# Kernel tuning notes

Measured on AMD Instinct MI355X. Metric: run time of the kernel, lower is better.

Reference implementation:

```python
import jax, jax.numpy as jnp
import numpy as np

NUM_FREQ = 32
MAX_POS = 10000.0
COORD_DIM = 3
EMB_DIM = COORD_DIM * NUM_FREQ * 2  # 192
KIN = 2 * EMB_DIM                   # 384
C = 32
T = 4
N_Y = 50000
N_X = 32768
K = 8
E = N_X * K
MLP_DIMS = [KIN, 128, 256, 128, C]


def sinusoidal_embed(p):
    # transformer-style sinusoidal embedding: [n, d] -> [n, d*NUM_FREQ*2]
    freqs = (1.0 / MAX_POS) ** (jnp.arange(NUM_FREQ, dtype=p.dtype) / NUM_FREQ)
    ang = p[..., None] * freqs                       # [n, d, nf]
    emb = jnp.stack([jnp.sin(ang), jnp.cos(ang)], axis=-1)  # [n, d, nf, 2]
    return emb.reshape(p.shape[0], -1)


def setup_inputs() -> dict:
    key = jax.random.key(0)
    ks = jax.random.split(key, 16)
    inp = {
        "y": jax.random.uniform(ks[0], (N_Y, COORD_DIM), dtype=jnp.float32),
        "x": jax.random.uniform(ks[1], (N_X, COORD_DIM), dtype=jnp.float32),
        "f_y": jax.random.normal(ks[2], (T, N_Y, C), dtype=jnp.float32),
        "neighbors_index": jax.random.randint(ks[3], (E,), 0, N_Y, dtype=jnp.int64),
    }
    # channel MLP params: 384 -> 128 -> 256 -> 128 -> 32, gelu between layers
    for i in range(4):
        fan_in, fan_out = MLP_DIMS[i], MLP_DIMS[i + 1]
        s = 1.0 / np.sqrt(fan_in)
        inp[f"W{i}"] = jax.random.uniform(ks[4 + 2 * i], (fan_in, fan_out), jnp.float32, -s, s)
        inp[f"b{i}"] = jax.random.uniform(ks[5 + 2 * i], (fan_out,), jnp.float32, -s, s)
    return inp


def reference(y, x, f_y, neighbors_index, W0, b0, W1, b1, W2, b2, W3, b3):
    n_x = x.shape[0]
    k = neighbors_index.shape[0] // n_x
    y_emb = sinusoidal_embed(y)            # [n_y, 192]
    x_emb = sinusoidal_embed(x)            # [n_x, 192]
    rep = y_emb[neighbors_index]           # [E, 192] gather per edge
    slf = jnp.repeat(x_emb, k, axis=0)     # [E, 192] query embedding per edge
    h = jnp.concatenate([rep, slf], axis=-1)  # [E, 384]
    h = jax.nn.gelu(h @ W0 + b0)
    h = jax.nn.gelu(h @ W1 + b1)
    h = jax.nn.gelu(h @ W2 + b2)
    kern = h @ W3 + b3                     # [E, C] kernel values
    in_feat = f_y[:, neighbors_index, :]   # [T, E, C] gathered source features
    prod = kern[None, :, :] * in_feat      # linear transform: k(x,y) * f(y)
    # reduction='sum' over each query's neighborhood (uniform K segments)
    out = prod.reshape(f_y.shape[0], n_x, k, -1).sum(axis=2)  # [T, n_x, C]
    return out
```

## Files before the change

kernel.cpp:

```cpp
#include <hip/hip_runtime.h>
#include <stdint.h>

#define EMB_DIM 192
#define CDIM 32
#define TDIM 4
#define N_Y 50000
#define N_X 32768
#define KNBR 8
#define ECNT (N_X*KNBR)

#define H1S 134
#define H2S 262
#define KS  33
#define ES  200

#define PREP_TW 272
#define PREP_Y0 PREP_TW
#define PREP_X0 (PREP_TW + 782)
#define PREP_NB (PREP_TW + 782 + 512)

typedef __attribute__((ext_vector_type(8))) short bf16x8;
typedef __attribute__((ext_vector_type(4))) float f32x4;

static __device__ __forceinline__ short f2bf(float f){
  unsigned u = __float_as_uint(f);
  return (short)((u + 0x7FFFu) >> 16);
}
static __device__ __forceinline__ unsigned pk_bf16(float lo, float hi){
  return ((__float_as_uint(lo) + 0x7FFFu) >> 16) |
         ((((__float_as_uint(hi) + 0x7FFFu) >> 16)) << 16);
}
static __device__ __forceinline__ float geluf(float x){
  float x2 = x * x;
  float u  = __builtin_fmaf(0.044715f, x2, 1.0f);
  float p  = x * -1.5957691216057308f;
  float e  = __expf(p * u);
  return x * __builtin_amdgcn_rcpf(1.0f + e);
}

__global__ __launch_bounds__(256, 2) void prep_all(
    const float* __restrict__ ypts, const float* __restrict__ xpts,
    const float* __restrict__ W0, const float* __restrict__ b0,
    const float* __restrict__ W1, const float* __restrict__ W2,
    const float* __restrict__ W3,
    short* __restrict__ w1t, short* __restrict__ w2t, short* __restrict__ w3t,
    short* __restrict__ c_y, float* __restrict__ c_x)
{
  const int tid = threadIdx.x;
  if (blockIdx.x < PREP_TW) {
    int id = blockIdx.x * 256 + tid;
    if (id < 32768) {
      int n = id >> 7, k = id & 127;
      w1t[id] = f2bf(W1[k * 256 + n]);
    } else if (id < 65536) {
      int loc = id - 32768; int n = loc >> 8, k = loc & 255;
      w2t[loc] = f2bf(W2[k * 128 + n]);
    } else if (id < 69632) {
      int loc = id - 65536; int n = loc >> 7, k = loc & 127;
      w3t[loc] = f2bf(W3[k * 32 + n]);
    }
    return;
  }

  __shared__ __attribute__((aligned(16))) short s_e[64 * ES];
  const bool isY = blockIdx.x < PREP_X0;
  const int row0 = isY ? (blockIdx.x - PREP_Y0) * 64 : (blockIdx.x - PREP_X0) * 64;
  const int wave = tid >> 6, lane = tid & 63;
  const int quad = lane >> 4, l15 = lane & 15;
  const float* W0h = W0 + (isY ? 0 : 192 * 128);

  short bv[2][48];
  #pragma unroll
  for (int nt = 0; nt < 2; ++nt) {
    int n = wave * 32 + nt * 16 + l15;
    #pragma unroll
    for (int ch = 0; ch < 6; ++ch)
      #pragma unroll
      for (int j = 0; j < 8; ++j)
        bv[nt][ch * 8 + j] = f2bf(W0h[(size_t)(ch * 32 + quad * 8 + j) * 128 + n]);
  }

  {
    const int r = tid >> 2, q = tid & 3;
    const int grow = row0 + r;
    const bool valid = isY ? (grow < N_Y) : true;
    const float* src = isY ? (ypts + (size_t)grow * 3) : (xpts + (size_t)grow * 3);
    float c[3] = {0.f, 0.f, 0.f};
    if (valid) { c[0] = src[0]; c[1] = src[1]; c[2] = src[2]; }
    #pragma unroll
    for (int j = 0; j < 24; ++j) {
      int p = q * 24 + j;
      int d = p >> 5, i = p & 31;
      float f = __expf(-0.28782313662425575f * (float)i);
      float rev = c[d] * f * 0.15915494309189535f;
      float s  = __builtin_amdgcn_sinf(rev);
      float co = __builtin_amdgcn_cosf(rev);
      *(unsigned*)&s_e[r * ES + d * 64 + 2 * i] = pk_bf16(s, co);
    }
  }
  __syncthreads();

  f32x4 acc[4][2];
  #pragma unroll
  for (int mt = 0; mt < 4; ++mt)
    #pragma unroll
    for (int nt = 0; nt < 2; ++nt) acc[mt][nt] = (f32x4){0.f, 0.f, 0.f, 0.f};
  #pragma unroll
  for (int ch = 0; ch < 6; ++ch) {
    bf16x8 a[4];
    #pragma unroll
    for (int mt = 0; mt < 4; ++mt)
      a[mt] = *(const bf16x8*)&s_e[(mt * 16 + l15) * ES + ch * 32 + quad * 8];
    #pragma unroll
    for (int mt = 0; mt < 4; ++mt)
      #pragma unroll
      for (int nt = 0; nt < 2; ++nt)
        acc[mt][nt] = __builtin_amdgcn_mfma_f32_16x16x32_bf16(
            a[mt], *(const bf16x8*)&bv[nt][ch * 8], acc[mt][nt], 0, 0, 0);
  }
  #pragma unroll
  for (int nt = 0; nt < 2; ++nt) {
    int col = wave * 32 + nt * 16 + l15;
    float bias = isY ? 0.f : b0[col];
    #pragma unroll
    for (int mt = 0; mt < 4; ++mt)
      #pragma unroll
      for (int rg = 0; rg < 4; ++rg) {
        int grow = row0 + mt * 16 + quad * 4 + rg;
        if (isY) { if (grow < N_Y) c_y[(size_t)grow * 128 + col] = f2bf(acc[mt][nt][rg]); }
        else     { c_x[(size_t)grow * 128 + col] = acc[mt][nt][rg] + bias; }
      }
  }
}

__global__ __launch_bounds__(256, 3) void fused_edge(
    const short* __restrict__ c_y, const float* __restrict__ c_x,
    const int* __restrict__ nidx, const float* __restrict__ f_y,
    const short* __restrict__ w1t, const float* __restrict__ b1,
    const short* __restrict__ w2t, const float* __restrict__ b2,
    const short* __restrict__ w3t, const float* __restrict__ b3,
    float* __restrict__ out)
{
  __shared__ __attribute__((aligned(16))) char smem[50688];
  short* s_h2   = (short*)smem;
  float* s_kern = (float*)smem;
  short* s_h1   = (short*)(smem + 33536);

  const int tid  = threadIdx.x;
  const int e0   = blockIdx.x * 64;
  const int wave = tid >> 6, lane = tid & 63;
  const int quad = lane >> 4, l15 = lane & 15;

  {
    const int r = tid >> 2, q = tid & 3;
    const int idx = nidx[e0 + r];
    const uint4*  cyp = (const uint4*)(c_y + (size_t)idx * 128 + q * 32);
    const float4* cxp = (const float4*)(c_x + (size_t)((e0 + r) >> 3) * 128 + q * 32);
    uint4  cyv[4];
    float4 cxv[8];
    #pragma unroll
    for (int i = 0; i < 4; ++i) cyv[i] = cyp[i];
    #pragma unroll
    for (int i = 0; i < 8; ++i) cxv[i] = cxp[i];
    const float* cxa = (const float*)cxv;
    const unsigned* cya = (const unsigned*)cyv;
    unsigned pk[16];
    #pragma unroll
    for (int jj = 0; jj < 16; ++jj) {
      unsigned u = cya[jj];
      float lo = __uint_as_float(u << 16)         + cxa[2 * jj];
      float hi = __uint_as_float(u & 0xffff0000u) + cxa[2 * jj + 1];
      pk[jj] = pk_bf16(geluf(lo), geluf(hi));
    }
    uint4* dst = (uint4*)&s_h1[r * H1S + q * 32];
    #pragma unroll
    for (int jj = 0; jj < 4; ++jj)
      dst[jj] = *(uint4*)&pk[jj * 4];
  }
  __syncthreads();

  {
    f32x4 acc1[4][4];
    #pragma unroll
    for (int mt = 0; mt < 4; ++mt)
      #pragma unroll
      for (int nt = 0; nt < 4; ++nt) acc1[mt][nt] = (f32x4){0.f, 0.f, 0.f, 0.f};
    #pragma unroll
    for (int ch = 0; ch < 4; ++ch) {
      bf16x8 a[4], b[4];
      #pragma unroll
      for (int mt = 0; mt < 4; ++mt)
        a[mt] = *(const bf16x8*)&s_h1[(mt * 16 + l15) * H1S + ch * 32 + quad * 8];
      #pragma unroll
      for (int nt = 0; nt < 4; ++nt)
        b[nt] = *(const bf16x8*)&w1t[(size_t)(wave * 64 + nt * 16 + l15) * 128 + ch * 32 + quad * 8];
      #pragma unroll
      for (int mt = 0; mt < 4; ++mt)
        #pragma unroll
        for (int nt = 0; nt < 4; ++nt)
          acc1[mt][nt] = __builtin_amdgcn_mfma_f32_16x16x32_bf16(a[mt], b[nt], acc1[mt][nt], 0, 0, 0);
    }
    #pragma unroll
    for (int nt = 0; nt < 4; ++nt) {
      int col = wave * 64 + nt * 16 + l15;
      float bias = b1[col];
      #pragma unroll
      for (int mt = 0; mt < 4; ++mt)
        #pragma unroll
        for (int rg = 0; rg < 4; ++rg) {
          int row = mt * 16 + quad * 4 + rg;
          s_h2[row * H2S + col] = f2bf(geluf(acc1[mt][nt][rg] + bias));
        }
    }
  }
  __syncthreads();

  {
    f32x4 acc2[4][2];
    #pragma unroll
    for (int mt = 0; mt < 4; ++mt)
      #pragma unroll
      for (int nt = 0; nt < 2; ++nt) acc2[mt][nt] = (f32x4){0.f, 0.f, 0.f, 0.f};
    #pragma unroll
    for (int ch = 0; ch < 8; ++ch) {
      bf16x8 a[4], b[2];
      #pragma unroll
      for (int mt = 0; mt < 4; ++mt)
        a[mt] = *(const bf16x8*)&s_h2[(mt * 16 + l15) * H2S + ch * 32 + quad * 8];
      #pragma unroll
      for (int nt = 0; nt < 2; ++nt)
        b[nt] = *(const bf16x8*)&w2t[(size_t)(wave * 32 + nt * 16 + l15) * 256 + ch * 32 + quad * 8];
      #pragma unroll
      for (int mt = 0; mt < 4; ++mt)
        #pragma unroll
        for (int nt = 0; nt < 2; ++nt)
          acc2[mt][nt] = __builtin_amdgcn_mfma_f32_16x16x32_bf16(a[mt], b[nt], acc2[mt][nt], 0, 0, 0);
    }
    #pragma unroll
    for (int nt = 0; nt < 2; ++nt) {
      int col = wave * 32 + nt * 16 + l15;
      float bias = b2[col];
      #pragma unroll
      for (int mt = 0; mt < 4; ++mt)
        #pragma unroll
        for (int rg = 0; rg < 4; ++rg) {
          int row = mt * 16 + quad * 4 + rg;
          s_h1[row * H1S + col] = f2bf(geluf(acc2[mt][nt][rg] + bias));
        }
    }
  }
  __syncthreads();

  {
    f32x4 acc3[2];
    acc3[0] = (f32x4){0.f, 0.f, 0.f, 0.f};
    acc3[1] = (f32x4){0.f, 0.f, 0.f, 0.f};
    #pragma unroll
    for (int ch = 0; ch < 4; ++ch) {
      bf16x8 a3 = *(const bf16x8*)&s_h1[(wave * 16 + l15) * H1S + ch * 32 + quad * 8];
      #pragma unroll
      for (int nt = 0; nt < 2; ++nt) {
        bf16x8 b3f = *(const bf16x8*)&w3t[(size_t)(nt * 16 + l15) * 128 + ch * 32 + quad * 8];
        acc3[nt] = __builtin_amdgcn_mfma_f32_16x16x32_bf16(a3, b3f, acc3[nt], 0, 0, 0);
      }
    }
    #pragma unroll
    for (int nt = 0; nt < 2; ++nt) {
      int col = nt * 16 + l15;
      float bias = b3[col];
      #pragma unroll
      for (int rg = 0; rg < 4; ++rg) {
        int row = wave * 16 + quad * 4 + rg;
        s_kern[row * KS + col] = acc3[nt][rg] + bias;
      }
    }
  }
  __syncthreads();

  {
    const int xloc = tid >> 5;
    const int c    = tid & 31;
    float acc[TDIM] = {0.f, 0.f, 0.f, 0.f};
    const int ebase = xloc * 8;
    #pragma unroll
    for (int j = 0; j < KNBR; ++j) {
      float kv = s_kern[(ebase + j) * KS + c];
      int idx = nidx[e0 + ebase + j];
      const float* fp = f_y + (size_t)idx * CDIM + c;
      #pragma unroll
      for (int t = 0; t < TDIM; ++t)
        acc[t] += kv * fp[(size_t)t * N_Y * CDIM];
    }
    const int xg = blockIdx.x * 8 + xloc;
    #pragma unroll
    for (int t = 0; t < TDIM; ++t)
      out[((size_t)t * N_X + xg) * CDIM + c] = acc[t];
  }
}

extern "C" void kernel_launch(void* const* d_in, const int* in_sizes, int n_in,
                              void* d_out, int out_size, void* d_ws, size_t ws_size,
                              hipStream_t stream)
{
  const float* y   = (const float*)d_in[0];
  const float* x   = (const float*)d_in[1];
  const float* f_y = (const float*)d_in[2];
  const int*  nidx = (const int*)d_in[3];
  const float* W0 = (const float*)d_in[4];  const float* b0 = (const float*)d_in[5];
  const float* W1 = (const float*)d_in[6];  const float* b1 = (const float*)d_in[7];
  const float* W2 = (const float*)d_in[8];  const float* b2 = (const float*)d_in[9];
  const float* W3 = (const float*)d_in[10]; const float* b3 = (const float*)d_in[11];

  char* ws = (char*)d_ws;
  short* c_y  = (short*)(ws + 0);
  float* c_x  = (float*)(ws + 12800000);
  short* w1t  = (short*)(ws + 29577216);
  short* w2t  = (short*)(ws + 29642752);
  short* w3t  = (short*)(ws + 29708288);

  hipLaunchKernelGGL(prep_all, dim3(PREP_NB), dim3(256), 0, stream,
                     y, x, W0, b0, W1, W2, W3, w1t, w2t, w3t, c_y, c_x);
  hipLaunchKernelGGL(fused_edge, dim3(ECNT / 64), dim3(256), 0, stream,
                     c_y, c_x, nidx, f_y, w1t, b1, w2t, b2, w3t, b3, (float*)d_out);
}
```

Measured before the change: 239.4 us.

## Prefetch f_y gathers and MLP weight fragments early to overlap latency

The random f_y gathers for the final reduction are now issued at kernel start and held in registers (32 floats per thread) across the whole MLP. The per-layer weight fragments are loaded into registers ahead of each MFMA loop, and the next layer's weights are issued before the current layer's GELU epilogue. The aim is to hide global-memory latency behind MFMA compute. The cost is much higher register pressure under launch_bounds(256,3), which may cause spills or lower occupancy.

```diff
diff --git a/kernel.cpp b/kernel.cpp
--- a/kernel.cpp
+++ b/kernel.cpp
@@ -151,17 +151,40 @@
   const int wave = tid >> 6, lane = tid & 63;
   const int quad = lane >> 4, l15 = lane & 15;
 
+  const int xloc = tid >> 5;
+  const int cc   = tid & 31;
+  int fidx[KNBR];
+  #pragma unroll
+  for (int j = 0; j < KNBR; ++j) fidx[j] = nidx[e0 + xloc * 8 + j];
+
+  const int r = tid >> 2, q = tid & 3;
+  const int idx = nidx[e0 + r];
+  const uint4*  cyp = (const uint4*)(c_y + (size_t)idx * 128 + q * 32);
+  const float4* cxp = (const float4*)(c_x + (size_t)((e0 + r) >> 3) * 128 + q * 32);
+  uint4  cyv[4];
+  float4 cxv[8];
+  #pragma unroll
+  for (int i = 0; i < 4; ++i) cyv[i] = cyp[i];
+  #pragma unroll
+  for (int i = 0; i < 8; ++i) cxv[i] = cxp[i];
+
+  bf16x8 b1f[4][4];
+  #pragma unroll
+  for (int ch = 0; ch < 4; ++ch)
+    #pragma unroll
+    for (int nt = 0; nt < 4; ++nt)
+      b1f[ch][nt] = *(const bf16x8*)&w1t[(size_t)(wave * 64 + nt * 16 + l15) * 128 + ch * 32 + quad * 8];
+
+  float fv[KNBR][TDIM];
+  #pragma unroll
+  for (int j = 0; j < KNBR; ++j) {
+    const float* fp = f_y + (size_t)fidx[j] * CDIM + cc;
+    #pragma unroll
+    for (int t = 0; t < TDIM; ++t)
+      fv[j][t] = fp[(size_t)t * (N_Y * CDIM)];
+  }
+
   {
-    const int r = tid >> 2, q = tid & 3;
-    const int idx = nidx[e0 + r];
-    const uint4*  cyp = (const uint4*)(c_y + (size_t)idx * 128 + q * 32);
-    const float4* cxp = (const float4*)(c_x + (size_t)((e0 + r) >> 3) * 128 + q * 32);
-    uint4  cyv[4];
-    float4 cxv[8];
-    #pragma unroll
-    for (int i = 0; i < 4; ++i) cyv[i] = cyp[i];
-    #pragma unroll
-    for (int i = 0; i < 8; ++i) cxv[i] = cxp[i];
     const float* cxa = (const float*)cxv;
     const unsigned* cya = (const unsigned*)cyv;
     unsigned pk[16];
@@ -179,75 +202,81 @@
   }
   __syncthreads();
 
-  {
-    f32x4 acc1[4][4];
-    #pragma unroll
-    for (int mt = 0; mt < 4; ++mt)
-      #pragma unroll
-      for (int nt = 0; nt < 4; ++nt) acc1[mt][nt] = (f32x4){0.f, 0.f, 0.f, 0.f};
-    #pragma unroll
-    for (int ch = 0; ch < 4; ++ch) {
-      bf16x8 a[4], b[4];
-      #pragma unroll
-      for (int mt = 0; mt < 4; ++mt)
-        a[mt] = *(const bf16x8*)&s_h1[(mt * 16 + l15) * H1S + ch * 32 + quad * 8];
+  f32x4 acc1[4][4];
+  #pragma unroll
+  for (int mt = 0; mt < 4; ++mt)
+    #pragma unroll
+    for (int nt = 0; nt < 4; ++nt) acc1[mt][nt] = (f32x4){0.f, 0.f, 0.f, 0.f};
+  #pragma unroll
+  for (int ch = 0; ch < 4; ++ch) {
+    bf16x8 a[4];
+    #pragma unroll
+    for (int mt = 0; mt < 4; ++mt)
+      a[mt] = *(const bf16x8*)&s_h1[(mt * 16 + l15) * H1S + ch * 32 + quad * 8];
+    #pragma unroll
+    for (int mt = 0; mt < 4; ++mt)
       #pragma unroll
       for (int nt = 0; nt < 4; ++nt)
-        b[nt] = *(const bf16x8*)&w1t[(size_t)(wave * 64 + nt * 16 + l15) * 128 + ch * 32 + quad * 8];
-      #pragma unroll
-      for (int mt = 0; mt < 4; ++mt)
-        #pragma unroll
-        for (int nt = 0; nt < 4; ++nt)
-          acc1[mt][nt] = __builtin_amdgcn_mfma_f32_16x16x32_bf16(a[mt], b[nt], acc1[mt][nt], 0, 0, 0);
-    }
-    #pragma unroll
-    for (int nt = 0; nt < 4; ++nt) {
-      int col = wave * 64 + nt * 16 + l15;
-      float bias = b1[col];
-      #pragma unroll
-      for (int mt = 0; mt < 4; ++mt)
-        #pragma unroll
-        for (int rg = 0; rg < 4; ++rg) {
-          int row = mt * 16 + quad * 4 + rg;
-          s_h2[row * H2S + col] = f2bf(geluf(acc1[mt][nt][rg] + bias));
-        }
-    }
-  }
-  __syncthreads();
-
-  {
-    f32x4 acc2[4][2];
-    #pragma unroll
-    for (int mt = 0; mt < 4; ++mt)
-      #pragma unroll
-      for (int nt = 0; nt < 2; ++nt) acc2[mt][nt] = (f32x4){0.f, 0.f, 0.f, 0.f};
-    #pragma unroll
-    for (int ch = 0; ch < 8; ++ch) {
-      bf16x8 a[4], b[2];
-      #pragma unroll
-      for (int mt = 0; mt < 4; ++mt)
-        a[mt] = *(const bf16x8*)&s_h2[(mt * 16 + l15) * H2S + ch * 32 + quad * 8];
+        acc1[mt][nt] = __builtin_amdgcn_mfma_f32_16x16x32_bf16(a[mt], b1f[ch][nt], acc1[mt][nt], 0, 0, 0);
+  }
+
+  bf16x8 b2f[8][2];
+  #pragma unroll
+  for (int ch = 0; ch < 8; ++ch)
+    #pragma unroll
+    for (int nt = 0; nt < 2; ++nt)
+      b2f[ch][nt] = *(const bf16x8*)&w2t[(size_t)(wave * 32 + nt * 16 + l15) * 256 + ch * 32 + quad * 8];
+
+  #pragma unroll
+  for (int nt = 0; nt < 4; ++nt) {
+    int col = wave * 64 + nt * 16 + l15;
+    float bias = b1[col];
+    #pragma unroll
+    for (int mt = 0; mt < 4; ++mt)
+      #pragma unroll
+      for (int rg = 0; rg < 4; ++rg) {
+        int row = mt * 16 + quad * 4 + rg;
+        s_h2[row * H2S + col] = f2bf(geluf(acc1[mt][nt][rg] + bias));
+      }
+  }
+  __syncthreads();
+
+  f32x4 acc2[4][2];
+  #pragma unroll
+  for (int mt = 0; mt < 4; ++mt)
+    #pragma unroll
+    for (int nt = 0; nt < 2; ++nt) acc2[mt][nt] = (f32x4){0.f, 0.f, 0.f, 0.f};
+  #pragma unroll
+  for (int ch = 0; ch < 8; ++ch) {
+    bf16x8 a[4];
+    #pragma unroll
+    for (int mt = 0; mt < 4; ++mt)
+      a[mt] = *(const bf16x8*)&s_h2[(mt * 16 + l15) * H2S + ch * 32 + quad * 8];
+    #pragma unroll
+    for (int mt = 0; mt < 4; ++mt)
       #pragma unroll
       for (int nt = 0; nt < 2; ++nt)
-        b[nt] = *(const bf16x8*)&w2t[(size_t)(wave * 32 + nt * 16 + l15) * 256 + ch * 32 + quad * 8];
-      #pragma unroll
-      for (int mt = 0; mt < 4; ++mt)
-        #pragma unroll
-        for (int nt = 0; nt < 2; ++nt)
-          acc2[mt][nt] = __builtin_amdgcn_mfma_f32_16x16x32_bf16(a[mt], b[nt], acc2[mt][nt], 0, 0, 0);
-    }
-    #pragma unroll
-    for (int nt = 0; nt < 2; ++nt) {
-      int col = wave * 32 + nt * 16 + l15;
-      float bias = b2[col];
-      #pragma unroll
-      for (int mt = 0; mt < 4; ++mt)
-        #pragma unroll
-        for (int rg = 0; rg < 4; ++rg) {
-          int row = mt * 16 + quad * 4 + rg;
-          s_h1[row * H1S + col] = f2bf(geluf(acc2[mt][nt][rg] + bias));
-        }
-    }
+        acc2[mt][nt] = __builtin_amdgcn_mfma_f32_16x16x32_bf16(a[mt], b2f[ch][nt], acc2[mt][nt], 0, 0, 0);
+  }
+
+  bf16x8 b3f[4][2];
+  #pragma unroll
+  for (int ch = 0; ch < 4; ++ch)
+    #pragma unroll
+    for (int nt = 0; nt < 2; ++nt)
+      b3f[ch][nt] = *(const bf16x8*)&w3t[(size_t)(nt * 16 + l15) * 128 + ch * 32 + quad * 8];
+
+  #pragma unroll
+  for (int nt = 0; nt < 2; ++nt) {
+    int col = wave * 32 + nt * 16 + l15;
+    float bias = b2[col];
+    #pragma unroll
+    for (int mt = 0; mt < 4; ++mt)
+      #pragma unroll
+      for (int rg = 0; rg < 4; ++rg) {
+        int row = mt * 16 + quad * 4 + rg;
+        s_h1[row * H1S + col] = f2bf(geluf(acc2[mt][nt][rg] + bias));
+      }
   }
   __syncthreads();
 
@@ -259,10 +288,8 @@
     for (int ch = 0; ch < 4; ++ch) {
       bf16x8 a3 = *(const bf16x8*)&s_h1[(wave * 16 + l15) * H1S + ch * 32 + quad * 8];
       #pragma unroll
-      for (int nt = 0; nt < 2; ++nt) {
-        bf16x8 b3f = *(const bf16x8*)&w3t[(size_t)(nt * 16 + l15) * 128 + ch * 32 + quad * 8];
-        acc3[nt] = __builtin_amdgcn_mfma_f32_16x16x32_bf16(a3, b3f, acc3[nt], 0, 0, 0);
-      }
+      for (int nt = 0; nt < 2; ++nt)
+        acc3[nt] = __builtin_amdgcn_mfma_f32_16x16x32_bf16(a3, b3f[ch][nt], acc3[nt], 0, 0, 0);
     }
     #pragma unroll
     for (int nt = 0; nt < 2; ++nt) {
@@ -278,23 +305,18 @@
   __syncthreads();
 
   {
-    const int xloc = tid >> 5;
-    const int c    = tid & 31;
     float acc[TDIM] = {0.f, 0.f, 0.f, 0.f};
-    const int ebase = xloc * 8;
     #pragma unroll
     for (int j = 0; j < KNBR; ++j) {
-      float kv = s_kern[(ebase + j) * KS + c];
-      int idx = nidx[e0 + ebase + j];
-      const float* fp = f_y + (size_t)idx * CDIM + c;
+      float kv = s_kern[(xloc * 8 + j) * KS + cc];
       #pragma unroll
       for (int t = 0; t < TDIM; ++t)
-        acc[t] += kv * fp[(size_t)t * N_Y * CDIM];
+        acc[t] += kv * fv[j][t];
     }
     const int xg = blockIdx.x * 8 + xloc;
     #pragma unroll
     for (int t = 0; t < TDIM; ++t)
-      out[((size_t)t * N_X + xg) * CDIM + c] = acc[t];
+      out[((size_t)t * N_X + xg) * CDIM + cc] = acc[t];
   }
 }
 
```

Measured after the change: 249.9 us. 4.4% more time.

## Double fused_edge block to 512 threads, splitting each stage's work across eight waves

Applied to the files above, without the earlier changes.

The fused edge kernel now runs 512 threads (8 waves) per 64-edge tile instead of 256. Every stage is repartitioned: the h1 build uses 8 threads per row, layers 1 and 2 give each wave half as many output columns, layer 3 splits M and N tiles across waves, and the final reduction splits the T dimension across two thread halves. The aim is fewer accumulator registers per thread and more waves per CU to hide gather and MFMA latency. In exchange, each wave issues fewer MFMAs per A-fragment load, so LDS reads of the activations are duplicated across more waves.

```diff
diff --git a/kernel.cpp b/kernel.cpp
--- a/kernel.cpp
+++ b/kernel.cpp
@@ -133,7 +133,7 @@
   }
 }
 
-__global__ __launch_bounds__(256, 3) void fused_edge(
+__global__ __launch_bounds__(512, 4) void fused_edge(
     const short* __restrict__ c_y, const float* __restrict__ c_x,
     const int* __restrict__ nidx, const float* __restrict__ f_y,
     const short* __restrict__ w1t, const float* __restrict__ b1,
@@ -152,57 +152,56 @@
   const int quad = lane >> 4, l15 = lane & 15;
 
   {
-    const int r = tid >> 2, q = tid & 3;
+    const int r = tid >> 3, q = tid & 7;
     const int idx = nidx[e0 + r];
-    const uint4*  cyp = (const uint4*)(c_y + (size_t)idx * 128 + q * 32);
-    const float4* cxp = (const float4*)(c_x + (size_t)((e0 + r) >> 3) * 128 + q * 32);
-    uint4  cyv[4];
-    float4 cxv[8];
-    #pragma unroll
-    for (int i = 0; i < 4; ++i) cyv[i] = cyp[i];
-    #pragma unroll
-    for (int i = 0; i < 8; ++i) cxv[i] = cxp[i];
+    const uint4*  cyp = (const uint4*)(c_y + (size_t)idx * 128 + q * 16);
+    const float4* cxp = (const float4*)(c_x + (size_t)((e0 + r) >> 3) * 128 + q * 16);
+    uint4  cyv[2];
+    float4 cxv[4];
+    #pragma unroll
+    for (int i = 0; i < 2; ++i) cyv[i] = cyp[i];
+    #pragma unroll
+    for (int i = 0; i < 4; ++i) cxv[i] = cxp[i];
     const float* cxa = (const float*)cxv;
     const unsigned* cya = (const unsigned*)cyv;
-    unsigned pk[16];
-    #pragma unroll
-    for (int jj = 0; jj < 16; ++jj) {
+    unsigned pk[8];
+    #pragma unroll
+    for (int jj = 0; jj < 8; ++jj) {
       unsigned u = cya[jj];
       float lo = __uint_as_float(u << 16)         + cxa[2 * jj];
       float hi = __uint_as_float(u & 0xffff0000u) + cxa[2 * jj + 1];
       pk[jj] = pk_bf16(geluf(lo), geluf(hi));
     }
-    uint4* dst = (uint4*)&s_h1[r * H1S + q * 32];
-    #pragma unroll
-    for (int jj = 0; jj < 4; ++jj)
-      dst[jj] = *(uint4*)&pk[jj * 4];
-  }
-  __syncthreads();
-
-  {
-    f32x4 acc1[4][4];
+    uint4* dst = (uint4*)&s_h1[r * H1S + q * 16];
+    dst[0] = *(uint4*)&pk[0];
+    dst[1] = *(uint4*)&pk[4];
+  }
+  __syncthreads();
+
+  {
+    f32x4 acc1[4][2];
     #pragma unroll
     for (int mt = 0; mt < 4; ++mt)
       #pragma unroll
-      for (int nt = 0; nt < 4; ++nt) acc1[mt][nt] = (f32x4){0.f, 0.f, 0.f, 0.f};
+      for (int nt = 0; nt < 2; ++nt) acc1[mt][nt] = (f32x4){0.f, 0.f, 0.f, 0.f};
     #pragma unroll
     for (int ch = 0; ch < 4; ++ch) {
-      bf16x8 a[4], b[4];
+      bf16x8 a[4], b[2];
       #pragma unroll
       for (int mt = 0; mt < 4; ++mt)
         a[mt] = *(const bf16x8*)&s_h1[(mt * 16 + l15) * H1S + ch * 32 + quad * 8];
       #pragma unroll
-      for (int nt = 0; nt < 4; ++nt)
-        b[nt] = *(const bf16x8*)&w1t[(size_t)(wave * 64 + nt * 16 + l15) * 128 + ch * 32 + quad * 8];
+      for (int nt = 0; nt < 2; ++nt)
+        b[nt] = *(const bf16x8*)&w1t[(size_t)(wave * 32 + nt * 16 + l15) * 128 + ch * 32 + quad * 8];
       #pragma unroll
       for (int mt = 0; mt < 4; ++mt)
         #pragma unroll
-        for (int nt = 0; nt < 4; ++nt)
+        for (int nt = 0; nt < 2; ++nt)
           acc1[mt][nt] = __builtin_amdgcn_mfma_f32_16x16x32_bf16(a[mt], b[nt], acc1[mt][nt], 0, 0, 0);
     }
     #pragma unroll
-    for (int nt = 0; nt < 4; ++nt) {
-      int col = wave * 64 + nt * 16 + l15;
+    for (int nt = 0; nt < 2; ++nt) {
+      int col = wave * 32 + nt * 16 + l15;
       float bias = b1[col];
       #pragma unroll
       for (int mt = 0; mt < 4; ++mt)
@@ -216,85 +215,75 @@
   __syncthreads();
 
   {
-    f32x4 acc2[4][2];
-    #pragma unroll
-    for (int mt = 0; mt < 4; ++mt)
-      #pragma unroll
-      for (int nt = 0; nt < 2; ++nt) acc2[mt][nt] = (f32x4){0.f, 0.f, 0.f, 0.f};
+    f32x4 acc2[4];
+    #pragma unroll
+    for (int mt = 0; mt < 4; ++mt) acc2[mt] = (f32x4){0.f, 0.f, 0.f, 0.f};
     #pragma unroll
     for (int ch = 0; ch < 8; ++ch) {
-      bf16x8 a[4], b[2];
+      bf16x8 a[4], b;
       #pragma unroll
       for (int mt = 0; mt < 4; ++mt)
         a[mt] = *(const bf16x8*)&s_h2[(mt * 16 + l15) * H2S + ch * 32 + quad * 8];
-      #pragma unroll
-      for (int nt = 0; nt < 2; ++nt)
-        b[nt] = *(const bf16x8*)&w2t[(size_t)(wave * 32 + nt * 16 + l15) * 256 + ch * 32 + quad * 8];
-      #pragma unroll
-      for (int mt = 0; mt < 4; ++mt)
-        #pragma unroll
-        for (int nt = 0; nt < 2; ++nt)
-          acc2[mt][nt] = __builtin_amdgcn_mfma_f32_16x16x32_bf16(a[mt], b[nt], acc2[mt][nt], 0, 0, 0);
-    }
-    #pragma unroll
-    for (int nt = 0; nt < 2; ++nt) {
-      int col = wave * 32 + nt * 16 + l15;
+      b = *(const bf16x8*)&w2t[(size_t)(wave * 16 + l15) * 256 + ch * 32 + quad * 8];
+      #pragma unroll
+      for (int mt = 0; mt < 4; ++mt)
+        acc2[mt] = __builtin_amdgcn_mfma_f32_16x16x32_bf16(a[mt], b, acc2[mt], 0, 0, 0);
+    }
+    {
+      int col = wave * 16 + l15;
       float bias = b2[col];
       #pragma unroll
       for (int mt = 0; mt < 4; ++mt)
         #pragma unroll
         for (int rg = 0; rg < 4; ++rg) {
           int row = mt * 16 + quad * 4 + rg;
-          s_h1[row * H1S + col] = f2bf(geluf(acc2[mt][nt][rg] + bias));
+          s_h1[row * H1S + col] = f2bf(geluf(acc2[mt][rg] + bias));
         }
     }
   }
   __syncthreads();
 
   {
-    f32x4 acc3[2];
-    acc3[0] = (f32x4){0.f, 0.f, 0.f, 0.f};
-    acc3[1] = (f32x4){0.f, 0.f, 0.f, 0.f};
+    const int mh = wave & 3;
+    const int nh = wave >> 2;
+    f32x4 acc3 = (f32x4){0.f, 0.f, 0.f, 0.f};
     #pragma unroll
     for (int ch = 0; ch < 4; ++ch) {
-      bf16x8 a3 = *(const bf16x8*)&s_h1[(wave * 16 + l15) * H1S + ch * 32 + quad * 8];
-      #pragma unroll
-      for (int nt = 0; nt < 2; ++nt) {
-        bf16x8 b3f = *(const bf16x8*)&w3t[(size_t)(nt * 16 + l15) * 128 + ch * 32 + quad * 8];
-        acc3[nt] = __builtin_amdgcn_mfma_f32_16x16x32_bf16(a3, b3f, acc3[nt], 0, 0, 0);
+      bf16x8 a3  = *(const bf16x8*)&s_h1[(mh * 16 + l15) * H1S + ch * 32 + quad * 8];
+      bf16x8 b3f = *(const bf16x8*)&w3t[(size_t)(nh * 16 + l15) * 128 + ch * 32 + quad * 8];
+      acc3 = __builtin_amdgcn_mfma_f32_16x16x32_bf16(a3, b3f, acc3, 0, 0, 0);
+    }
+    {
+      int col = nh * 16 + l15;
+      float bias = b3[col];
+      #pragma unroll
+      for (int rg = 0; rg < 4; ++rg) {
+        int row = mh * 16 + quad * 4 + rg;
+        s_kern[row * KS + col] = acc3[rg] + bias;
       }
     }
-    #pragma unroll
-    for (int nt = 0; nt < 2; ++nt) {
-      int col = nt * 16 + l15;
-      float bias = b3[col];
-      #pragma unroll
-      for (int rg = 0; rg < 4; ++rg) {
-        int row = wave * 16 + quad * 4 + rg;
-        s_kern[row * KS + col] = acc3[nt][rg] + bias;
-      }
-    }
-  }
-  __syncthreads();
-
-  {
-    const int xloc = tid >> 5;
-    const int c    = tid & 31;
-    float acc[TDIM] = {0.f, 0.f, 0.f, 0.f};
+  }
+  __syncthreads();
+
+  {
+    const int cc   = tid & 31;
+    const int xloc = (tid >> 5) & 7;
+    const int th   = tid >> 8;
+    float acc[2] = {0.f, 0.f};
     const int ebase = xloc * 8;
     #pragma unroll
     for (int j = 0; j < KNBR; ++j) {
-      float kv = s_kern[(ebase + j) * KS + c];
+      float kv = s_kern[(ebase + j) * KS + cc];
       int idx = nidx[e0 + ebase + j];
-      const float* fp = f_y + (size_t)idx * CDIM + c;
-      #pragma unroll
-      for (int t = 0; t < TDIM; ++t)
-        acc[t] += kv * fp[(size_t)t * N_Y * CDIM];
+      const float* fp = f_y + (size_t)idx * CDIM + cc;
+      #pragma unroll
+      for (int tt = 0; tt < 2; ++tt)
+        acc[tt] += kv * fp[(size_t)(th * 2 + tt) * (N_Y * CDIM)];
     }
     const int xg = blockIdx.x * 8 + xloc;
     #pragma unroll
-    for (int t = 0; t < TDIM; ++t)
-      out[((size_t)t * N_X + xg) * CDIM + c] = acc[t];
+    for (int tt = 0; tt < 2; ++tt)
+      out[((size_t)(th * 2 + tt) * N_X + xg) * CDIM + cc] = acc[tt];
   }
 }
 
@@ -320,6 +309,6 @@
 
   hipLaunchKernelGGL(prep_all, dim3(PREP_NB), dim3(256), 0, stream,
                      y, x, W0, b0, W1, W2, W3, w1t, w2t, w3t, c_y, c_x);
-  hipLaunchKernelGGL(fused_edge, dim3(ECNT / 64), dim3(256), 0, stream,
+  hipLaunchKernelGGL(fused_edge, dim3(ECNT / 64), dim3(512), 0, stream,
                      c_y, c_x, nidx, f_y, w1t, b1, w2t, b2, w3t, b3, (float*)d_out);
 }
```

After: 311.9 us. 30.3% more time.
